# Kernel optimization log

Measured on AMD Instinct MI355X. Metric: run time of the kernel, lower is better.

## Reference

```python
import jax, jax.numpy as jnp
import numpy as np

K_SEL = 8        # selection budget K
R_ITER = 1       # fixed-point refinement steps r
LAM = 0.5        # lam
MAX_PROXY = 16   # max_proxy_points
KNN_K = 1        # knn_k = max(1, r)


def knn_stats(x, k):
    # x: [B,N,D] -> [B,N,4] stats of k nearest-neighbor distances (self excluded)
    sq = jnp.sum(x * x, axis=-1)
    d2 = sq[:, :, None] + sq[:, None, :] - 2.0 * jnp.einsum('bnd,bmd->bnm', x, x)
    n = x.shape[1]
    d2 = d2 + jnp.eye(n, dtype=x.dtype) * 1e9  # mask self-distance
    neg_vals, _ = jax.lax.top_k(-d2, k)        # k smallest distances
    d = jnp.sqrt(jnp.maximum(-neg_vals, 0.0))  # [B,N,k]
    return jnp.stack([d.mean(-1), d.min(-1), d.max(-1), d.std(-1)], axis=-1)


def build_structural(x, selection_weights=None, knn_k=KNN_K):
    feats = jnp.concatenate([x, knn_stats(x, knn_k)], axis=-1)
    if selection_weights is not None:
        feats = jnp.concatenate([feats, selection_weights[..., None]], axis=-1)
    return feats


def feature_similarity(f):
    fn = f / (jnp.linalg.norm(f, axis=-1, keepdims=True) + 1e-8)
    return jnp.einsum('bnd,bmd->bnm', fn, fn)


def soft_selector(saliency, similarity, log_temp):
    # SoftSelectorProxy.forward
    temp = jnp.clip(jnp.exp(log_temp), 0.1, 10.0)
    y = jax.nn.sigmoid((saliency / (2.0 * LAM) - 0.5) / temp)

    def rescale(y):
        budget = jnp.clip(y.sum(axis=1, keepdims=True), 1e-6, None)
        return y * jnp.minimum(K_SEL / budget, 1.0)

    y = rescale(y)
    for _ in range(R_ITER):
        overlap = jnp.einsum('bnm,bm->bn', similarity, y)
        y = rescale(y / (1.0 + overlap))
    return y


def setup_inputs() -> dict:
    key = jax.random.key(0)
    ks = jax.random.split(key, 8)
    B, N, D, H = 8, 2048, 32, 64
    K_LIFT, D_MODEL = 16, 256
    ANCHOR = D + 4  # structural_feature_dim(input_dim, include_selection=False)
    s = 0.02
    return {
        'x': jax.random.normal(ks[0], (B, N, D), dtype=jnp.float32),
        'log_temp': jnp.zeros((), dtype=jnp.float32),  # init_temperature=1.0
        'W1': jax.random.normal(ks[1], (D, H), dtype=jnp.float32) * s,
        'b1': jnp.zeros((H,), dtype=jnp.float32),
        'W2': jax.random.normal(ks[2], (H, 1), dtype=jnp.float32) * s,
        'b2': jnp.zeros((1,), dtype=jnp.float32),
        'mu': jnp.zeros((ANCHOR,), dtype=jnp.float32),
        'sigma': jnp.ones((ANCHOR,), dtype=jnp.float32),
        'Wl': jax.random.normal(ks[3], (ANCHOR, K_LIFT), dtype=jnp.float32) * s,
        'bl': jnp.zeros((K_LIFT,), dtype=jnp.float32),
        'Wp': jax.random.normal(ks[4], (K_LIFT, D_MODEL), dtype=jnp.float32) * s,
        'bp': jnp.zeros((D_MODEL,), dtype=jnp.float32),
    }


def reference(x, log_temp, W1, b1, W2, b2, mu, sigma, Wl, bl, Wp, bp):
    # CausalEventModel: per-point MLP saliency head
    h = jax.nn.relu(jnp.einsum('bnd,dh->bnh', x, W1) + b1)
    saliency = (jnp.einsum('bnh,ho->bno', h, W2) + b2)[..., 0]  # [B,N]

    structural = build_structural(x, selection_weights=saliency)
    similarity = feature_similarity(structural)                  # [B,N,N]
    y_star = soft_selector(saliency, similarity, log_temp)       # [B,N]

    dense = build_structural(x, selection_weights=None)          # [B,N,anchor]
    lifted = jnp.tanh(jnp.einsum('bna,ak->bnk', (dense - mu) / sigma, Wl) + bl)

    N = lifted.shape[1]
    K_eff = min(N, MAX_PROXY)
    _, top_idx = jax.lax.top_k(y_star, K_eff)                    # [B,K_eff]
    cloud = jnp.take_along_axis(lifted, top_idx[..., None], axis=1)  # [B,K_eff,k]
    tokens = jnp.einsum('bkc,cd->bkd', cloud, Wp) + bp           # [B,K_eff,d_model]
    return tokens, y_star
```

## Files before the change

kernel.cpp:

```cpp
#include <hip/hip_runtime.h>
#include <math.h>

#define B 8
#define N 2048
#define DIM 32
#define HID 64
#define KLIFT 16
#define DMODEL 256
#define KPROXY 16
#define KSEL 8.0f

typedef float f32x4 __attribute__((ext_vector_type(4)));
typedef short bf16x8 __attribute__((ext_vector_type(8)));

__device__ inline unsigned short f2bf(float f) {
  unsigned u = __float_as_uint(f);
  unsigned r = (u + 0x7FFFu + ((u >> 16) & 1u)) >> 16;
  return (unsigned short)r;
}
__device__ inline float bf2f(unsigned short s) {
  return __uint_as_float(((unsigned)s) << 16);
}

__global__ __launch_bounds__(64) void k_prep(
    const float* __restrict__ x, const float* __restrict__ W1,
    const float* __restrict__ b1, const float* __restrict__ W2,
    const float* __restrict__ b2, float* __restrict__ sal,
    float* __restrict__ sq, unsigned short* __restrict__ Xhi,
    unsigned short* __restrict__ Xlo, unsigned* __restrict__ nnd2) {
  __shared__ float sW1[DIM * HID];
  __shared__ float sW2[HID], sb1[HID];
  int t = threadIdx.x;
  {
    const float4* s4 = (const float4*)W1;
    float4* d4 = (float4*)sW1;
    for (int i = t; i < DIM * HID / 4; i += 64) d4[i] = s4[i];
    sW2[t] = W2[t]; sb1[t] = b1[t];
  }
  __syncthreads();
  int p = blockIdx.x * 64 + t;
  nnd2[p] = 0x7F7F7F7Fu;
  float xr[DIM];
  const float4* xp = (const float4*)(x + (size_t)p * DIM);
#pragma unroll
  for (int i = 0; i < DIM / 4; i++) {
    float4 v = xp[i];
    xr[4 * i + 0] = v.x; xr[4 * i + 1] = v.y; xr[4 * i + 2] = v.z; xr[4 * i + 3] = v.w;
  }
  float s = 0.f;
#pragma unroll
  for (int d = 0; d < DIM; d++) s = fmaf(xr[d], xr[d], s);
  sq[p] = s;
  float h[HID];
#pragma unroll
  for (int j = 0; j < HID; j++) h[j] = sb1[j];
  for (int d = 0; d < DIM; d++) {
    float xv = xr[d];
    const float4* wrow = (const float4*)(&sW1[d * HID]);
#pragma unroll
    for (int j4 = 0; j4 < HID / 4; j4++) {
      float4 w = wrow[j4];
      h[4 * j4 + 0] = fmaf(xv, w.x, h[4 * j4 + 0]);
      h[4 * j4 + 1] = fmaf(xv, w.y, h[4 * j4 + 1]);
      h[4 * j4 + 2] = fmaf(xv, w.z, h[4 * j4 + 2]);
      h[4 * j4 + 3] = fmaf(xv, w.w, h[4 * j4 + 3]);
    }
  }
  float acc = b2[0];
#pragma unroll
  for (int j = 0; j < HID; j++) acc = fmaf(fmaxf(h[j], 0.f), sW2[j], acc);
  sal[p] = acc;
  int bb = p >> 11, n = p & (N - 1);
  int tile = n >> 4, c = n & 15;
  size_t tb = ((size_t)(bb * 128 + tile)) * 64;
#pragma unroll
  for (int g = 0; g < 4; g++) {
    bf16x8 hv, lv;
#pragma unroll
    for (int j = 0; j < 8; j++) {
      float v = xr[g * 8 + j];
      unsigned short hb = f2bf(v);
      hv[j] = (short)hb;
      lv[j] = (short)f2bf(v - bf2f(hb));
    }
    size_t off = (tb + (size_t)g * 16 + c) * 8;
    *(bf16x8*)(Xhi + off) = hv;
    *(bf16x8*)(Xlo + off) = lv;
  }
}

__global__ __launch_bounds__(256) void k_nnd(
    const unsigned short* __restrict__ Xhi, const unsigned short* __restrict__ Xlo,
    const float* __restrict__ sq, unsigned* __restrict__ nnd2) {
  int bid = blockIdx.x;
  int bb = bid >> 6;
  int nch = (bid >> 2) & 15;
  int mq = bid & 3;
  int t = threadIdx.x;
  int w = t >> 6, lane = t & 63;
  int c = lane & 15, g = lane >> 4;
  __shared__ unsigned short ldsH[32 * 512];
  __shared__ unsigned short ldsL[32 * 512];
  __shared__ float ssq[512];
  {
    size_t base = ((size_t)(bb * 128 + mq * 32)) * 512;
    const float4* srcH = (const float4*)(Xhi + base);
    const float4* srcL = (const float4*)(Xlo + base);
    float4* dH = (float4*)ldsH;
    float4* dL = (float4*)ldsL;
    for (int i = t; i < 32 * 512 / 8; i += 256) { dH[i] = srcH[i]; dL[i] = srcL[i]; }
    ssq[t] = sq[bb * N + mq * 512 + t];
    ssq[t + 256] = sq[bb * N + mq * 512 + t + 256];
  }
  int nt0 = nch * 8 + w * 2, nt1 = nt0 + 1;
  bf16x8 ah0 = *(const bf16x8*)(Xhi + (((size_t)(bb * 128 + nt0)) * 64 + lane) * 8);
  bf16x8 al0 = *(const bf16x8*)(Xlo + (((size_t)(bb * 128 + nt0)) * 64 + lane) * 8);
  bf16x8 ah1 = *(const bf16x8*)(Xhi + (((size_t)(bb * 128 + nt1)) * 64 + lane) * 8);
  bf16x8 al1 = *(const bf16x8*)(Xlo + (((size_t)(bb * 128 + nt1)) * 64 + lane) * 8);
  __syncthreads();
  float mn0[4] = {1e30f, 1e30f, 1e30f, 1e30f};
  float mn1[4] = {1e30f, 1e30f, 1e30f, 1e30f};
  for (int tt = 0; tt < 32; tt++) {
    bf16x8 bh = ((const bf16x8*)(ldsH + tt * 512))[lane];
    bf16x8 bl2 = ((const bf16x8*)(ldsL + tt * 512))[lane];
    f32x4 a0 = {0.f, 0.f, 0.f, 0.f};
    f32x4 a1 = {0.f, 0.f, 0.f, 0.f};
    a0 = __builtin_amdgcn_mfma_f32_16x16x32_bf16(ah0, bh, a0, 0, 0, 0);
    a1 = __builtin_amdgcn_mfma_f32_16x16x32_bf16(ah1, bh, a1, 0, 0, 0);
    a0 = __builtin_amdgcn_mfma_f32_16x16x32_bf16(ah0, bl2, a0, 0, 0, 0);
    a1 = __builtin_amdgcn_mfma_f32_16x16x32_bf16(ah1, bl2, a1, 0, 0, 0);
    a0 = __builtin_amdgcn_mfma_f32_16x16x32_bf16(al0, bh, a0, 0, 0, 0);
    a1 = __builtin_amdgcn_mfma_f32_16x16x32_bf16(al1, bh, a1, 0, 0, 0);
    float sm = ssq[tt * 16 + c];
    int mtg = mq * 32 + tt;
    bool d0 = (mtg == nt0), d1 = (mtg == nt1);
#pragma unroll
    for (int r = 0; r < 4; r++) {
      float v0 = fmaf(-2.f, a0[r], sm);
      float v1 = fmaf(-2.f, a1[r], sm);
      if (d0 && c == 4 * g + r) v0 = 1e30f;
      if (d1 && c == 4 * g + r) v1 = 1e30f;
      mn0[r] = fminf(mn0[r], v0);
      mn1[r] = fminf(mn1[r], v1);
    }
  }
#pragma unroll
  for (int off = 1; off <= 8; off <<= 1) {
#pragma unroll
    for (int r = 0; r < 4; r++) {
      mn0[r] = fminf(mn0[r], __shfl_xor(mn0[r], off));
      mn1[r] = fminf(mn1[r], __shfl_xor(mn1[r], off));
    }
  }
  if (c == 0) {
#pragma unroll
    for (int r = 0; r < 4; r++) {
      int n0 = nt0 * 16 + 4 * g + r;
      float v = fmaxf(sq[bb * N + n0] + mn0[r], 0.f);
      atomicMin(&nnd2[bb * N + n0], __float_as_uint(v));
      int n1 = nt1 * 16 + 4 * g + r;
      v = fmaxf(sq[bb * N + n1] + mn1[r], 0.f);
      atomicMin(&nnd2[bb * N + n1], __float_as_uint(v));
    }
  }
}

__global__ __launch_bounds__(512) void k_post(
    const float* __restrict__ x, const float* __restrict__ sal,
    const float* __restrict__ sq, const unsigned* __restrict__ nnd2,
    const float* __restrict__ logt, const float* __restrict__ mu,
    const float* __restrict__ sigma, const float* __restrict__ Wl,
    const float* __restrict__ bl, const float* __restrict__ Wp,
    const float* __restrict__ bp, float* __restrict__ tok,
    float* __restrict__ ystar) {
  int b = blockIdx.x, t = threadIdx.x;
  int lane = t & 63, wid = t >> 6;
  __shared__ float yv[N];
  __shared__ float red[8];
  __shared__ float gpart[8][34];
  __shared__ float gfin[34];
  __shared__ float bsh[2];
  __shared__ float candv[128];
  __shared__ int candi[128];
  __shared__ int tix[KPROXY];
  __shared__ float sz[KPROXY][36];

  float temp = fminf(fmaxf(expf(logt[0]), 0.1f), 10.f);
  float xr[4][DIM], sl[4], dv[4], nrm[4], y0[4];
#pragma unroll
  for (int i = 0; i < 4; i++) {
    int n = t + 512 * i;
    size_t base = (size_t)b * N + n;
    const float4* p4 = (const float4*)(x + base * DIM);
#pragma unroll
    for (int cc = 0; cc < 8; cc++) {
      float4 v = p4[cc];
      xr[i][4 * cc + 0] = v.x; xr[i][4 * cc + 1] = v.y;
      xr[i][4 * cc + 2] = v.z; xr[i][4 * cc + 3] = v.w;
    }
    sl[i] = sal[base];
    dv[i] = sqrtf(__uint_as_float(nnd2[base]));
    nrm[i] = sqrtf(sq[base] + 3.f * dv[i] * dv[i] + sl[i] * sl[i]) + 1e-8f;
    y0[i] = 1.f / (1.f + expf(-((sl[i] - 0.5f) / temp)));
  }
  float part = y0[0] + y0[1] + y0[2] + y0[3];
#pragma unroll
  for (int off = 32; off >= 1; off >>= 1) part += __shfl_xor(part, off);
  if (lane == 0) red[wid] = part;
  __syncthreads();
  if (t == 0) { float s = 0; for (int ww = 0; ww < 8; ww++) s += red[ww]; bsh[0] = s; }
  __syncthreads();
  float scale1 = fminf(KSEL / fmaxf(bsh[0], 1e-6f), 1.f);
  float y1[4];
#pragma unroll
  for (int i = 0; i < 4; i++) y1[i] = y0[i] * scale1;
  float gg[34];
  float c0 = y1[0] / nrm[0], c1 = y1[1] / nrm[1];
  float c2 = y1[2] / nrm[2], c3 = y1[3] / nrm[3];
#pragma unroll
  for (int d = 0; d < DIM; d++)
    gg[d] = c0 * xr[0][d] + c1 * xr[1][d] + c2 * xr[2][d] + c3 * xr[3][d];
  gg[32] = c0 * dv[0] + c1 * dv[1] + c2 * dv[2] + c3 * dv[3];
  gg[33] = c0 * sl[0] + c1 * sl[1] + c2 * sl[2] + c3 * sl[3];
#pragma unroll
  for (int k2 = 0; k2 < 34; k2++) {
    float v = gg[k2];
#pragma unroll
    for (int off = 32; off >= 1; off >>= 1) v += __shfl_xor(v, off);
    gg[k2] = v;
  }
  if (lane == 0) {
#pragma unroll
    for (int k2 = 0; k2 < 34; k2++) gpart[wid][k2] = gg[k2];
  }
  __syncthreads();
  if (t < 34) {
    float s = 0;
    for (int ww = 0; ww < 8; ww++) s += gpart[ww][t];
    gfin[t] = s;
  }
  __syncthreads();
  float y2[4];
#pragma unroll
  for (int i = 0; i < 4; i++) {
    float ov = 0.f;
#pragma unroll
    for (int d = 0; d < DIM; d++) ov = fmaf(xr[i][d], gfin[d], ov);
    ov += 3.f * dv[i] * gfin[32] + sl[i] * gfin[33];
    ov /= nrm[i];
    y2[i] = y1[i] / (1.f + ov);
  }
  float part2 = y2[0] + y2[1] + y2[2] + y2[3];
#pragma unroll
  for (int off = 32; off >= 1; off >>= 1) part2 += __shfl_xor(part2, off);
  if (lane == 0) red[wid] = part2;
  __syncthreads();
  if (t == 0) { float s = 0; for (int ww = 0; ww < 8; ww++) s += red[ww]; bsh[1] = s; }
  __syncthreads();
  float scale2 = fminf(KSEL / fmaxf(bsh[1], 1e-6f), 1.f);
#pragma unroll
  for (int i = 0; i < 4; i++) {
    int n = t + 512 * i;
    float ys = y2[i] * scale2;
    yv[n] = ys;
    ystar[(size_t)b * N + n] = ys;
  }
  __syncthreads();
  float lv0 = yv[wid * 256 + lane];        int li0 = wid * 256 + lane;
  float lv1 = yv[wid * 256 + 64 + lane];   int li1 = li0 + 64;
  float lv2 = yv[wid * 256 + 128 + lane];  int li2 = li0 + 128;
  float lv3 = yv[wid * 256 + 192 + lane];  int li3 = li0 + 192;
  for (int r = 0; r < KPROXY; r++) {
    float bv = lv0; int bi = li0;
    if (lv1 > bv) { bv = lv1; bi = li1; }
    if (lv2 > bv) { bv = lv2; bi = li2; }
    if (lv3 > bv) { bv = lv3; bi = li3; }
#pragma unroll
    for (int off = 1; off < 64; off <<= 1) {
      float ovv = __shfl_xor(bv, off);
      int oi = __shfl_xor(bi, off);
      if (ovv > bv || (ovv == bv && oi < bi)) { bv = ovv; bi = oi; }
    }
    if (lane == 0) { candv[wid * 16 + r] = bv; candi[wid * 16 + r] = bi; }
    if (li0 == bi) lv0 = -1e30f;
    if (li1 == bi) lv1 = -1e30f;
    if (li2 == bi) lv2 = -1e30f;
    if (li3 == bi) lv3 = -1e30f;
  }
  __syncthreads();
  if (wid == 0) {
    float cv0 = candv[lane], cv1 = candv[lane + 64];
    int ci0 = candi[lane], ci1 = candi[lane + 64];
    for (int r = 0; r < KPROXY; r++) {
      float bv = cv0; int bi = ci0;
      if (cv1 > bv || (cv1 == bv && ci1 < bi)) { bv = cv1; bi = ci1; }
#pragma unroll
      for (int off = 1; off < 64; off <<= 1) {
        float ovv = __shfl_xor(bv, off);
        int oi = __shfl_xor(bi, off);
        if (ovv > bv || (ovv == bv && oi < bi)) { bv = ovv; bi = oi; }
      }
      if (lane == 0) tix[r] = bi;
      if (ci0 == bi) cv0 = -1e30f;
      if (ci1 == bi) cv1 = -1e30f;
    }
  }
  __syncthreads();
  for (int it = 0; it < 2; it++) {
    int k = wid + 8 * it;
    int srow = tix[k];
    if (lane < 36) {
      float f;
      if (lane < 32) f = x[((size_t)b * N + srow) * DIM + lane];
      else if (lane < 35) f = sqrtf(__uint_as_float(nnd2[b * N + srow]));
      else f = 0.f;
      sz[k][lane] = (f - mu[lane]) / sigma[lane];
    }
    __syncthreads();
    float lf = 0.f;
    if (lane < KLIFT) {
      float a = bl[lane];
#pragma unroll
      for (int d = 0; d < 36; d++) a = fmaf(sz[k][d], Wl[d * KLIFT + lane], a);
      lf = tanhf(a);
    }
    float o0 = bp[lane], o1 = bp[lane + 64], o2 = bp[lane + 128], o3 = bp[lane + 192];
#pragma unroll
    for (int j = 0; j < KLIFT; j++) {
      float lj = __shfl(lf, j);
      const float* wr = Wp + j * DMODEL + lane;
      o0 = fmaf(lj, wr[0], o0);
      o1 = fmaf(lj, wr[64], o1);
      o2 = fmaf(lj, wr[128], o2);
      o3 = fmaf(lj, wr[192], o3);
    }
    float* tp = tok + ((size_t)b * KPROXY + k) * DMODEL + lane;
    tp[0] = o0; tp[64] = o1; tp[128] = o2; tp[192] = o3;
  }
}

extern "C" void kernel_launch(void* const* d_in, const int* in_sizes, int n_in,
                              void* d_out, int out_size, void* d_ws, size_t ws_size,
                              hipStream_t stream) {
  const float* x  = (const float*)d_in[0];
  const float* lt = (const float*)d_in[1];
  const float* W1 = (const float*)d_in[2];
  const float* b1 = (const float*)d_in[3];
  const float* W2 = (const float*)d_in[4];
  const float* b2 = (const float*)d_in[5];
  const float* mu = (const float*)d_in[6];
  const float* sg = (const float*)d_in[7];
  const float* Wl = (const float*)d_in[8];
  const float* bl = (const float*)d_in[9];
  const float* Wp = (const float*)d_in[10];
  const float* bp = (const float*)d_in[11];

  float* tok = (float*)d_out;
  float* ystar = tok + B * KPROXY * DMODEL;

  char* ws = (char*)d_ws;
  float* sal           = (float*)(ws);
  float* sq            = (float*)(ws + 65536);
  unsigned* nnd2       = (unsigned*)(ws + 131072);
  unsigned short* Xhi  = (unsigned short*)(ws + 196608);
  unsigned short* Xlo  = (unsigned short*)(ws + 196608 + 1048576);

  k_prep<<<B * N / 64, 64, 0, stream>>>(x, W1, b1, W2, b2, sal, sq, Xhi, Xlo, nnd2);
  k_nnd<<<512, 256, 0, stream>>>(Xhi, Xlo, sq, nnd2);
  k_post<<<B, 512, 0, stream>>>(x, sal, sq, nnd2, lt, mu, sg, Wl, bl, Wp, bp, tok, ystar);
}
```

Before: 64.41 us.

## Spread soft-selector reductions across many blocks instead of one block per batch

The first budget sum moves into the prep kernel as per-block partials. The nearest-neighbour kernel now scans all columns per tile, so it can write distances directly without atomics, and it also accumulates the weighted feature-sum partials. A new kernel computes the overlap and y2 across 64 blocks, leaving k_post with only the final rescale and top-k. This takes the heavy per-point work out of the 8-block post kernel, which underused the GPU. The cost is an extra launch, fewer nnd blocks (256 instead of 512), and repeated loads of the column tiles.

```diff
diff --git a/kernel.cpp b/kernel.cpp
--- a/kernel.cpp
+++ b/kernel.cpp
@@ -21,25 +21,30 @@
 __device__ inline float bf2f(unsigned short s) {
   return __uint_as_float(((unsigned)s) << 16);
 }
-
-__global__ __launch_bounds__(64) void k_prep(
+__device__ inline float clip_temp(float lt) {
+  return fminf(fmaxf(expf(lt), 0.1f), 10.f);
+}
+
+__global__ __launch_bounds__(256) void k_prep(
     const float* __restrict__ x, const float* __restrict__ W1,
     const float* __restrict__ b1, const float* __restrict__ W2,
-    const float* __restrict__ b2, float* __restrict__ sal,
-    float* __restrict__ sq, unsigned short* __restrict__ Xhi,
-    unsigned short* __restrict__ Xlo, unsigned* __restrict__ nnd2) {
+    const float* __restrict__ b2, const float* __restrict__ logt,
+    float* __restrict__ sal, float* __restrict__ sq,
+    unsigned short* __restrict__ Xhi, unsigned short* __restrict__ Xlo,
+    float* __restrict__ partials1) {
   __shared__ float sW1[DIM * HID];
   __shared__ float sW2[HID], sb1[HID];
+  __shared__ float red[4];
   int t = threadIdx.x;
+  int lane = t & 63, wid = t >> 6;
   {
     const float4* s4 = (const float4*)W1;
     float4* d4 = (float4*)sW1;
-    for (int i = t; i < DIM * HID / 4; i += 64) d4[i] = s4[i];
-    sW2[t] = W2[t]; sb1[t] = b1[t];
-  }
-  __syncthreads();
-  int p = blockIdx.x * 64 + t;
-  nnd2[p] = 0x7F7F7F7Fu;
+    for (int i = t; i < DIM * HID / 4; i += 256) d4[i] = s4[i];
+    if (t < HID) { sW2[t] = W2[t]; sb1[t] = b1[t]; }
+  }
+  __syncthreads();
+  int p = blockIdx.x * 256 + t;
   float xr[DIM];
   const float4* xp = (const float4*)(x + (size_t)p * DIM);
 #pragma unroll
@@ -70,6 +75,14 @@
 #pragma unroll
   for (int j = 0; j < HID; j++) acc = fmaf(fmaxf(h[j], 0.f), sW2[j], acc);
   sal[p] = acc;
+  float temp = clip_temp(logt[0]);
+  float y0 = 1.f / (1.f + expf(-((acc - 0.5f) / temp)));
+  float part = y0;
+#pragma unroll
+  for (int off = 32; off >= 1; off >>= 1) part += __shfl_xor(part, off);
+  if (lane == 0) red[wid] = part;
+  __syncthreads();
+  if (t == 0) partials1[blockIdx.x] = red[0] + red[1] + red[2] + red[3];
   int bb = p >> 11, n = p & (N - 1);
   int tile = n >> 4, c = n & 15;
   size_t tb = ((size_t)(bb * 128 + tile)) * 64;
@@ -91,84 +104,165 @@
 
 __global__ __launch_bounds__(256) void k_nnd(
     const unsigned short* __restrict__ Xhi, const unsigned short* __restrict__ Xlo,
-    const float* __restrict__ sq, unsigned* __restrict__ nnd2) {
+    const float* __restrict__ sq, const float* __restrict__ sal,
+    const float* __restrict__ x, const float* __restrict__ logt,
+    const float* __restrict__ partials1,
+    float* __restrict__ nnd2f, float* __restrict__ gpart) {
   int bid = blockIdx.x;
-  int bb = bid >> 6;
-  int nch = (bid >> 2) & 15;
-  int mq = bid & 3;
-  int t = threadIdx.x;
-  int w = t >> 6, lane = t & 63;
+  int bb = bid >> 5, nch = bid & 31;
+  int t = threadIdx.x, w = t >> 6, lane = t & 63;
   int c = lane & 15, g = lane >> 4;
+  int ntile = nch * 4 + w;
   __shared__ unsigned short ldsH[32 * 512];
   __shared__ unsigned short ldsL[32 * 512];
   __shared__ float ssq[512];
-  {
-    size_t base = ((size_t)(bb * 128 + mq * 32)) * 512;
+  __shared__ float dvs[64], cs[64];
+  __shared__ float gsh[8][32];
+  bf16x8 ah = *(const bf16x8*)(Xhi + (((size_t)(bb * 128 + ntile)) * 64 + lane) * 8);
+  bf16x8 al = *(const bf16x8*)(Xlo + (((size_t)(bb * 128 + ntile)) * 64 + lane) * 8);
+  float mn[4] = {1e30f, 1e30f, 1e30f, 1e30f};
+  for (int mc = 0; mc < 4; mc++) {
+    __syncthreads();
+    size_t base = ((size_t)(bb * 128 + mc * 32)) * 512;
     const float4* srcH = (const float4*)(Xhi + base);
     const float4* srcL = (const float4*)(Xlo + base);
     float4* dH = (float4*)ldsH;
     float4* dL = (float4*)ldsL;
-    for (int i = t; i < 32 * 512 / 8; i += 256) { dH[i] = srcH[i]; dL[i] = srcL[i]; }
-    ssq[t] = sq[bb * N + mq * 512 + t];
-    ssq[t + 256] = sq[bb * N + mq * 512 + t + 256];
-  }
-  int nt0 = nch * 8 + w * 2, nt1 = nt0 + 1;
-  bf16x8 ah0 = *(const bf16x8*)(Xhi + (((size_t)(bb * 128 + nt0)) * 64 + lane) * 8);
-  bf16x8 al0 = *(const bf16x8*)(Xlo + (((size_t)(bb * 128 + nt0)) * 64 + lane) * 8);
-  bf16x8 ah1 = *(const bf16x8*)(Xhi + (((size_t)(bb * 128 + nt1)) * 64 + lane) * 8);
-  bf16x8 al1 = *(const bf16x8*)(Xlo + (((size_t)(bb * 128 + nt1)) * 64 + lane) * 8);
-  __syncthreads();
-  float mn0[4] = {1e30f, 1e30f, 1e30f, 1e30f};
-  float mn1[4] = {1e30f, 1e30f, 1e30f, 1e30f};
-  for (int tt = 0; tt < 32; tt++) {
-    bf16x8 bh = ((const bf16x8*)(ldsH + tt * 512))[lane];
-    bf16x8 bl2 = ((const bf16x8*)(ldsL + tt * 512))[lane];
-    f32x4 a0 = {0.f, 0.f, 0.f, 0.f};
-    f32x4 a1 = {0.f, 0.f, 0.f, 0.f};
-    a0 = __builtin_amdgcn_mfma_f32_16x16x32_bf16(ah0, bh, a0, 0, 0, 0);
-    a1 = __builtin_amdgcn_mfma_f32_16x16x32_bf16(ah1, bh, a1, 0, 0, 0);
-    a0 = __builtin_amdgcn_mfma_f32_16x16x32_bf16(ah0, bl2, a0, 0, 0, 0);
-    a1 = __builtin_amdgcn_mfma_f32_16x16x32_bf16(ah1, bl2, a1, 0, 0, 0);
-    a0 = __builtin_amdgcn_mfma_f32_16x16x32_bf16(al0, bh, a0, 0, 0, 0);
-    a1 = __builtin_amdgcn_mfma_f32_16x16x32_bf16(al1, bh, a1, 0, 0, 0);
-    float sm = ssq[tt * 16 + c];
-    int mtg = mq * 32 + tt;
-    bool d0 = (mtg == nt0), d1 = (mtg == nt1);
+    for (int i = t; i < 2048; i += 256) { dH[i] = srcH[i]; dL[i] = srcL[i]; }
+    ssq[t] = sq[bb * N + mc * 512 + t];
+    ssq[t + 256] = sq[bb * N + mc * 512 + t + 256];
+    __syncthreads();
+    for (int tt = 0; tt < 32; tt++) {
+      bf16x8 bh = ((const bf16x8*)(ldsH + tt * 512))[lane];
+      bf16x8 bl2 = ((const bf16x8*)(ldsL + tt * 512))[lane];
+      f32x4 a0 = {0.f, 0.f, 0.f, 0.f};
+      a0 = __builtin_amdgcn_mfma_f32_16x16x32_bf16(ah, bh, a0, 0, 0, 0);
+      a0 = __builtin_amdgcn_mfma_f32_16x16x32_bf16(ah, bl2, a0, 0, 0, 0);
+      a0 = __builtin_amdgcn_mfma_f32_16x16x32_bf16(al, bh, a0, 0, 0, 0);
+      float sm = ssq[tt * 16 + c];
+      int mtg = mc * 32 + tt;
+      bool diag = (mtg == ntile);
+#pragma unroll
+      for (int r = 0; r < 4; r++) {
+        float v = fmaf(-2.f, a0[r], sm);
+        if (diag && c == 4 * g + r) v = 1e30f;
+        mn[r] = fminf(mn[r], v);
+      }
+    }
+  }
+#pragma unroll
+  for (int off = 1; off <= 8; off <<= 1) {
+#pragma unroll
+    for (int r = 0; r < 4; r++) mn[r] = fminf(mn[r], __shfl_xor(mn[r], off));
+  }
+  if (c == 0) {
 #pragma unroll
     for (int r = 0; r < 4; r++) {
-      float v0 = fmaf(-2.f, a0[r], sm);
-      float v1 = fmaf(-2.f, a1[r], sm);
-      if (d0 && c == 4 * g + r) v0 = 1e30f;
-      if (d1 && c == 4 * g + r) v1 = 1e30f;
-      mn0[r] = fminf(mn0[r], v0);
-      mn1[r] = fminf(mn1[r], v1);
-    }
-  }
-#pragma unroll
-  for (int off = 1; off <= 8; off <<= 1) {
-#pragma unroll
-    for (int r = 0; r < 4; r++) {
-      mn0[r] = fminf(mn0[r], __shfl_xor(mn0[r], off));
-      mn1[r] = fminf(mn1[r], __shfl_xor(mn1[r], off));
-    }
-  }
-  if (c == 0) {
-#pragma unroll
-    for (int r = 0; r < 4; r++) {
-      int n0 = nt0 * 16 + 4 * g + r;
-      float v = fmaxf(sq[bb * N + n0] + mn0[r], 0.f);
-      atomicMin(&nnd2[bb * N + n0], __float_as_uint(v));
-      int n1 = nt1 * 16 + 4 * g + r;
-      v = fmaxf(sq[bb * N + n1] + mn1[r], 0.f);
-      atomicMin(&nnd2[bb * N + n1], __float_as_uint(v));
-    }
-  }
+      int n0 = ntile * 16 + 4 * g + r;
+      float d2 = fmaxf(sq[bb * N + n0] + mn[r], 0.f);
+      nnd2f[bb * N + n0] = d2;
+      dvs[w * 16 + 4 * g + r] = sqrtf(d2);
+    }
+  }
+  __syncthreads();
+  float temp = clip_temp(logt[0]);
+  if (t < 64) {
+    int n = nch * 64 + t;
+    size_t basep = (size_t)bb * N + n;
+    float b1v = 0.f;
+    for (int j = 0; j < 8; j++) b1v += partials1[bb * 8 + j];
+    float scale1 = fminf(KSEL / fmaxf(b1v, 1e-6f), 1.f);
+    float sv = sal[basep];
+    float y0 = 1.f / (1.f + expf(-((sv - 0.5f) / temp)));
+    float y1 = y0 * scale1;
+    float dv = dvs[t];
+    float nrm = sqrtf(sq[basep] + 3.f * dv * dv + sv * sv) + 1e-8f;
+    float cn = y1 / nrm;
+    cs[t] = cn;
+    float v32 = cn * dv, v33 = cn * sv;
+#pragma unroll
+    for (int off = 32; off >= 1; off >>= 1) {
+      v32 += __shfl_xor(v32, off);
+      v33 += __shfl_xor(v33, off);
+    }
+    if (t == 0) {
+      gpart[(size_t)(bb * 32 + nch) * 36 + 32] = v32;
+      gpart[(size_t)(bb * 32 + nch) * 36 + 33] = v33;
+    }
+  }
+  __syncthreads();
+  int d = t & 31, pg = t >> 5;
+  float acc = 0.f;
+#pragma unroll
+  for (int i = 0; i < 8; i++)
+    acc = fmaf(cs[pg * 8 + i], x[((size_t)bb * N + nch * 64 + pg * 8 + i) * DIM + d], acc);
+  gsh[pg][d] = acc;
+  __syncthreads();
+  if (t < 32) {
+    float s = 0.f;
+#pragma unroll
+    for (int pgi = 0; pgi < 8; pgi++) s += gsh[pgi][t];
+    gpart[(size_t)(bb * 32 + nch) * 36 + t] = s;
+  }
+}
+
+__global__ __launch_bounds__(256) void k_c(
+    const float* __restrict__ x, const float* __restrict__ sal,
+    const float* __restrict__ sq, const float* __restrict__ nnd2f,
+    const float* __restrict__ logt, const float* __restrict__ partials1,
+    const float* __restrict__ gpart, float* __restrict__ partials2,
+    float* __restrict__ ystar) {
+  int bid = blockIdx.x;
+  int bb = bid >> 3, ch = bid & 7;
+  int t = threadIdx.x, lane = t & 63, wid = t >> 6;
+  __shared__ float gfin[34];
+  __shared__ float s1sh;
+  __shared__ float red[4];
+  if (t < 34) {
+    float s = 0.f;
+    for (int j = 0; j < 32; j++) s += gpart[(size_t)(bb * 32 + j) * 36 + t];
+    gfin[t] = s;
+  }
+  if (t == 40) {
+    float s = 0.f;
+    for (int j = 0; j < 8; j++) s += partials1[bb * 8 + j];
+    s1sh = fminf(KSEL / fmaxf(s, 1e-6f), 1.f);
+  }
+  __syncthreads();
+  float scale1 = s1sh;
+  int n = ch * 256 + t;
+  size_t base = (size_t)bb * N + n;
+  float temp = clip_temp(logt[0]);
+  float sv = sal[base];
+  float y0 = 1.f / (1.f + expf(-((sv - 0.5f) / temp)));
+  float y1 = y0 * scale1;
+  float dv = sqrtf(nnd2f[base]);
+  float nrm = sqrtf(sq[base] + 3.f * dv * dv + sv * sv) + 1e-8f;
+  const float4* p4 = (const float4*)(x + base * DIM);
+  float ov = 0.f;
+#pragma unroll
+  for (int cc = 0; cc < 8; cc++) {
+    float4 v = p4[cc];
+    ov = fmaf(v.x, gfin[4 * cc + 0], ov);
+    ov = fmaf(v.y, gfin[4 * cc + 1], ov);
+    ov = fmaf(v.z, gfin[4 * cc + 2], ov);
+    ov = fmaf(v.w, gfin[4 * cc + 3], ov);
+  }
+  ov += 3.f * dv * gfin[32] + sv * gfin[33];
+  ov /= nrm;
+  float y2 = y1 / (1.f + ov);
+  ystar[base] = y2;
+  float part = y2;
+#pragma unroll
+  for (int off = 32; off >= 1; off >>= 1) part += __shfl_xor(part, off);
+  if (lane == 0) red[wid] = part;
+  __syncthreads();
+  if (t == 0) partials2[bb * 8 + ch] = red[0] + red[1] + red[2] + red[3];
 }
 
 __global__ __launch_bounds__(512) void k_post(
-    const float* __restrict__ x, const float* __restrict__ sal,
-    const float* __restrict__ sq, const unsigned* __restrict__ nnd2,
-    const float* __restrict__ logt, const float* __restrict__ mu,
+    const float* __restrict__ x, const float* __restrict__ nnd2f,
+    const float* __restrict__ partials2, const float* __restrict__ mu,
     const float* __restrict__ sigma, const float* __restrict__ Wl,
     const float* __restrict__ bl, const float* __restrict__ Wp,
     const float* __restrict__ bp, float* __restrict__ tok,
@@ -176,94 +270,24 @@
   int b = blockIdx.x, t = threadIdx.x;
   int lane = t & 63, wid = t >> 6;
   __shared__ float yv[N];
-  __shared__ float red[8];
-  __shared__ float gpart[8][34];
-  __shared__ float gfin[34];
-  __shared__ float bsh[2];
+  __shared__ float bsh;
   __shared__ float candv[128];
   __shared__ int candi[128];
   __shared__ int tix[KPROXY];
   __shared__ float sz[KPROXY][36];
-
-  float temp = fminf(fmaxf(expf(logt[0]), 0.1f), 10.f);
-  float xr[4][DIM], sl[4], dv[4], nrm[4], y0[4];
+  if (t == 0) {
+    float s = 0.f;
+    for (int j = 0; j < 8; j++) s += partials2[b * 8 + j];
+    bsh = fminf(KSEL / fmaxf(s, 1e-6f), 1.f);
+  }
+  __syncthreads();
+  float scale2 = bsh;
 #pragma unroll
   for (int i = 0; i < 4; i++) {
     int n = t + 512 * i;
-    size_t base = (size_t)b * N + n;
-    const float4* p4 = (const float4*)(x + base * DIM);
-#pragma unroll
-    for (int cc = 0; cc < 8; cc++) {
-      float4 v = p4[cc];
-      xr[i][4 * cc + 0] = v.x; xr[i][4 * cc + 1] = v.y;
-      xr[i][4 * cc + 2] = v.z; xr[i][4 * cc + 3] = v.w;
-    }
-    sl[i] = sal[base];
-    dv[i] = sqrtf(__uint_as_float(nnd2[base]));
-    nrm[i] = sqrtf(sq[base] + 3.f * dv[i] * dv[i] + sl[i] * sl[i]) + 1e-8f;
-    y0[i] = 1.f / (1.f + expf(-((sl[i] - 0.5f) / temp)));
-  }
-  float part = y0[0] + y0[1] + y0[2] + y0[3];
-#pragma unroll
-  for (int off = 32; off >= 1; off >>= 1) part += __shfl_xor(part, off);
-  if (lane == 0) red[wid] = part;
-  __syncthreads();
-  if (t == 0) { float s = 0; for (int ww = 0; ww < 8; ww++) s += red[ww]; bsh[0] = s; }
-  __syncthreads();
-  float scale1 = fminf(KSEL / fmaxf(bsh[0], 1e-6f), 1.f);
-  float y1[4];
-#pragma unroll
-  for (int i = 0; i < 4; i++) y1[i] = y0[i] * scale1;
-  float gg[34];
-  float c0 = y1[0] / nrm[0], c1 = y1[1] / nrm[1];
-  float c2 = y1[2] / nrm[2], c3 = y1[3] / nrm[3];
-#pragma unroll
-  for (int d = 0; d < DIM; d++)
-    gg[d] = c0 * xr[0][d] + c1 * xr[1][d] + c2 * xr[2][d] + c3 * xr[3][d];
-  gg[32] = c0 * dv[0] + c1 * dv[1] + c2 * dv[2] + c3 * dv[3];
-  gg[33] = c0 * sl[0] + c1 * sl[1] + c2 * sl[2] + c3 * sl[3];
-#pragma unroll
-  for (int k2 = 0; k2 < 34; k2++) {
-    float v = gg[k2];
-#pragma unroll
-    for (int off = 32; off >= 1; off >>= 1) v += __shfl_xor(v, off);
-    gg[k2] = v;
-  }
-  if (lane == 0) {
-#pragma unroll
-    for (int k2 = 0; k2 < 34; k2++) gpart[wid][k2] = gg[k2];
-  }
-  __syncthreads();
-  if (t < 34) {
-    float s = 0;
-    for (int ww = 0; ww < 8; ww++) s += gpart[ww][t];
-    gfin[t] = s;
-  }
-  __syncthreads();
-  float y2[4];
-#pragma unroll
-  for (int i = 0; i < 4; i++) {
-    float ov = 0.f;
-#pragma unroll
-    for (int d = 0; d < DIM; d++) ov = fmaf(xr[i][d], gfin[d], ov);
-    ov += 3.f * dv[i] * gfin[32] + sl[i] * gfin[33];
-    ov /= nrm[i];
-    y2[i] = y1[i] / (1.f + ov);
-  }
-  float part2 = y2[0] + y2[1] + y2[2] + y2[3];
-#pragma unroll
-  for (int off = 32; off >= 1; off >>= 1) part2 += __shfl_xor(part2, off);
-  if (lane == 0) red[wid] = part2;
-  __syncthreads();
-  if (t == 0) { float s = 0; for (int ww = 0; ww < 8; ww++) s += red[ww]; bsh[1] = s; }
-  __syncthreads();
-  float scale2 = fminf(KSEL / fmaxf(bsh[1], 1e-6f), 1.f);
-#pragma unroll
-  for (int i = 0; i < 4; i++) {
-    int n = t + 512 * i;
-    float ys = y2[i] * scale2;
-    yv[n] = ys;
-    ystar[(size_t)b * N + n] = ys;
+    float y = ystar[(size_t)b * N + n] * scale2;
+    yv[n] = y;
+    ystar[(size_t)b * N + n] = y;
   }
   __syncthreads();
   float lv0 = yv[wid * 256 + lane];        int li0 = wid * 256 + lane;
@@ -312,7 +336,7 @@
     if (lane < 36) {
       float f;
       if (lane < 32) f = x[((size_t)b * N + srow) * DIM + lane];
-      else if (lane < 35) f = sqrtf(__uint_as_float(nnd2[b * N + srow]));
+      else if (lane < 35) f = sqrtf(nnd2f[b * N + srow]);
       else f = 0.f;
       sz[k][lane] = (f - mu[lane]) / sigma[lane];
     }
@@ -359,13 +383,17 @@
   float* ystar = tok + B * KPROXY * DMODEL;
 
   char* ws = (char*)d_ws;
-  float* sal           = (float*)(ws);
-  float* sq            = (float*)(ws + 65536);
-  unsigned* nnd2       = (unsigned*)(ws + 131072);
-  unsigned short* Xhi  = (unsigned short*)(ws + 196608);
-  unsigned short* Xlo  = (unsigned short*)(ws + 196608 + 1048576);
-
-  k_prep<<<B * N / 64, 64, 0, stream>>>(x, W1, b1, W2, b2, sal, sq, Xhi, Xlo, nnd2);
-  k_nnd<<<512, 256, 0, stream>>>(Xhi, Xlo, sq, nnd2);
-  k_post<<<B, 512, 0, stream>>>(x, sal, sq, nnd2, lt, mu, sg, Wl, bl, Wp, bp, tok, ystar);
-}
+  float* sal          = (float*)(ws);
+  float* sq           = (float*)(ws + 65536);
+  float* nnd2f        = (float*)(ws + 131072);
+  float* partials1    = (float*)(ws + 196608);
+  float* gpart        = (float*)(ws + 197120);
+  float* partials2    = (float*)(ws + 234496);
+  unsigned short* Xhi = (unsigned short*)(ws + 262144);
+  unsigned short* Xlo = (unsigned short*)(ws + 262144 + 1048576);
+
+  k_prep<<<B * N / 256, 256, 0, stream>>>(x, W1, b1, W2, b2, lt, sal, sq, Xhi, Xlo, partials1);
+  k_nnd<<<B * 32, 256, 0, stream>>>(Xhi, Xlo, sq, sal, x, lt, partials1, nnd2f, gpart);
+  k_c<<<B * 8, 256, 0, stream>>>(x, sal, sq, nnd2f, lt, partials1, gpart, partials2, ystar);
+  k_post<<<B, 512, 0, stream>>>(x, nnd2f, partials2, mu, sg, Wl, bl, Wp, bp, tok, ystar);
+}
```

Result: slower. 67.40 us (+4.6%).
